# Performance work log

Measured on AMD Instinct MI355X. Metric: run time of the kernel, lower is better.

The kernel has to match this reference:

```python
import jax, jax.numpy as jnp
import numpy as np

N, E, IN, HID, C = 100000, 1600000, 128, 64, 40
LN_EPS = 1e-5


def setup_inputs() -> dict:
    key = jax.random.key(0)
    ks = jax.random.split(key, 20)
    x = jax.random.normal(ks[0], (N, IN), dtype=jnp.float32)
    edge_index = jax.random.randint(ks[1], (2, E), 0, N, dtype=jnp.int64)
    def lin(k, fi, fo):
        s = 1.0 / np.sqrt(fi)
        return jax.random.uniform(k, (fi, fo), jnp.float32, -s, s)
    inp = {"x": x, "edge_index": edge_index}
    dims = [(IN, HID), (HID, HID), (HID, HID)]
    for i, (fi, fo) in enumerate(dims, 1):
        inp[f"W{i}"] = lin(ks[2 * i], fi, fo)
        inp[f"b{i}"] = jnp.zeros((fo,), jnp.float32)
        inp[f"g{i}"] = jnp.ones((fo,), jnp.float32)
        inp[f"t{i}"] = jnp.zeros((fo,), jnp.float32)
    inp["Wf"] = lin(ks[10], HID, C)
    inp["bf"] = jnp.zeros((C,), jnp.float32)
    return inp


def _layer_norm(h, g, t):
    mu = jnp.mean(h, axis=-1, keepdims=True)
    var = jnp.mean((h - mu) ** 2, axis=-1, keepdims=True)
    return g * (h - mu) * jax.lax.rsqrt(var + LN_EPS) + t


def reference(x, edge_index, W1, b1, g1, t1, W2, b2, g2, t2, W3, b3, g3, t3, Wf, bf):
    n = x.shape[0]
    src, dst = edge_index[0], edge_index[1]
    # GCN symmetric normalization (add_self_loops=False): deg = in-degree of dst
    deg = jax.ops.segment_sum(jnp.ones_like(dst, dtype=x.dtype), dst, num_segments=n)
    dinv = jnp.where(deg > 0, jax.lax.rsqrt(deg), 0.0)
    norm = dinv[src] * dinv[dst]  # [E]

    def gcn(h, W, b):
        hw = h @ W                                  # [n, out]
        msg = hw[src] * norm[:, None]               # [E, out] gather + scale
        return jax.ops.segment_sum(msg, dst, num_segments=n) + b

    h = x
    for W, b, g, t in ((W1, b1, g1, t1), (W2, b2, g2, t2), (W3, b3, g3, t3)):
        h = gcn(h, W, b)
        h = _layer_norm(h, g, t)
        h = jax.nn.relu(h)  # dropout is identity in eval mode
    logits = h @ Wf + bf
    return jax.nn.log_softmax(logits, axis=-1)
```

## Files before the change

kernel.cpp:

```cpp
#include <hip/hip_runtime.h>
#include <math.h>
#include <stdint.h>

#define LN_EPS 1e-5f
#define GRP_SHIFT 7
#define MAXBUK 1024
#define PCHUNK 4096

__device__ __forceinline__ unsigned short f2bf(float f) {
  unsigned int u = __float_as_uint(f);
  unsigned int r = u + 0x7fffu + ((u >> 16) & 1u);
  return (unsigned short)(r >> 16);
}
__device__ __forceinline__ float bfLo(unsigned v) { return __uint_as_float(v << 16); }
__device__ __forceinline__ float bfHi(unsigned v) { return __uint_as_float(v & 0xffff0000u); }

__global__ __launch_bounds__(1024) void k_bucket_count(const int* __restrict__ dst,
                                                       int* __restrict__ bcnt, int E, int NB) {
  __shared__ int hist[MAXBUK];
  int t = threadIdx.x;
  for (int i = t; i < NB; i += 1024) hist[i] = 0;
  __syncthreads();
  int e0 = blockIdx.x * PCHUNK;
  int e1 = min(e0 + PCHUNK, E);
#pragma unroll
  for (int j = 0; j < 4; ++j) {
    int i = e0 + t + j * 1024;
    if (i < e1) atomicAdd(&hist[dst[i] >> GRP_SHIFT], 1);
  }
  __syncthreads();
  for (int i = t; i < NB; i += 1024)
    if (hist[i]) atomicAdd(&bcnt[i], hist[i]);
}

__global__ __launch_bounds__(256) void k_bucket_scan(const int* __restrict__ cnt,
                                                     int* __restrict__ base,
                                                     int* __restrict__ cur, int NB) {
  __shared__ int ts[256];
  int t = threadIdx.x;
  int v[4];
  int s = 0;
#pragma unroll
  for (int j = 0; j < 4; ++j) { int i = t * 4 + j; v[j] = (i < NB) ? cnt[i] : 0; s += v[j]; }
  ts[t] = s;
  __syncthreads();
  for (int o = 1; o < 256; o <<= 1) {
    int x = (t >= o) ? ts[t - o] : 0;
    __syncthreads();
    ts[t] += x;
    __syncthreads();
  }
  int run = ts[t] - s;
#pragma unroll
  for (int j = 0; j < 4; ++j) {
    int i = t * 4 + j;
    if (i < NB) { base[i] = run; cur[i] = run; }
    run += v[j];
  }
  if (t == 255) base[NB] = run;
}

__global__ __launch_bounds__(1024) void k_partition(const int* __restrict__ src,
                                                    const int* __restrict__ dst,
                                                    int* __restrict__ bcur,
                                                    unsigned* __restrict__ pairs, int E, int NB) {
  __shared__ int hist[MAXBUK];
  __shared__ int base[MAXBUK];
  int t = threadIdx.x;
  for (int i = t; i < NB; i += 1024) hist[i] = 0;
  __syncthreads();
  int e0 = blockIdx.x * PCHUNK;
  int e1 = min(e0 + PCHUNK, E);
  int sv[4], dv[4], rk[4];
#pragma unroll
  for (int j = 0; j < 4; ++j) {
    int i = e0 + t + j * 1024;
    if (i < e1) {
      sv[j] = src[i];
      dv[j] = dst[i];
      rk[j] = atomicAdd(&hist[dv[j] >> GRP_SHIFT], 1);
    } else {
      dv[j] = -1;
    }
  }
  __syncthreads();
  for (int i = t; i < NB; i += 1024) {
    int c = hist[i];
    base[i] = c ? atomicAdd(&bcur[i], c) : 0;
  }
  __syncthreads();
#pragma unroll
  for (int j = 0; j < 4; ++j) {
    if (dv[j] >= 0) {
      int b = dv[j] >> GRP_SHIFT;
      pairs[base[b] + rk[j]] = ((unsigned)sv[j] << GRP_SHIFT) | (unsigned)(dv[j] & 127);
    }
  }
}

__global__ __launch_bounds__(256) void k_bucket_place(const unsigned* __restrict__ pairs,
                                                      const int* __restrict__ bbase,
                                                      int* __restrict__ offsets,
                                                      float* __restrict__ dinv,
                                                      int* __restrict__ csr, int N, int E) {
  __shared__ int cnt[128];
  __shared__ int sc[128];
  int t = threadIdx.x;
  int b = blockIdx.x;
  int node0 = b << GRP_SHIFT;
  if (t < 128) cnt[t] = 0;
  int beg = bbase[b], end = bbase[b + 1];
  if (b == 0 && t == 0) offsets[N] = E;
  __syncthreads();
  for (int i = beg + t; i < end; i += 256) atomicAdd(&cnt[pairs[i] & 127u], 1);
  __syncthreads();
  if (t < 128) sc[t] = cnt[t];
  __syncthreads();
  for (int o = 1; o < 128; o <<= 1) {
    int x = (t < 128 && t >= o) ? sc[t - o] : 0;
    __syncthreads();
    if (t < 128) sc[t] += x;
    __syncthreads();
  }
  if (t < 128) {
    int excl = sc[t] - cnt[t];
    int node = node0 + t;
    if (node < N) {
      offsets[node] = beg + excl;
      int d = cnt[t];
      dinv[node] = d > 0 ? rsqrtf((float)d) : 0.f;
    }
    sc[t] = beg + excl;
  }
  __syncthreads();
  for (int i = beg + t; i < end; i += 256) {
    unsigned pk = pairs[i];
    int pos = atomicAdd(&sc[pk & 127u], 1);
    csr[pos] = (int)(pk >> GRP_SHIFT);
  }
}

template <int K>
__global__ __launch_bounds__(256) void gemm_scale(const float* __restrict__ A,
                                                  const float* __restrict__ W,
                                                  const float* __restrict__ dinv,
                                                  unsigned short* __restrict__ out, int M) {
  __shared__ float xs[16][64];
  __shared__ float wsh[16][64];
  int t = threadIdx.x;
  int m0 = blockIdx.x * 64;
  int lm = t >> 2;
  int lk = (t & 3) << 2;
  int mr = (t & 15) << 2;
  int cc = (t >> 4) << 2;
  float acc[4][4] = {{0.f}};
  int gm = m0 + lm;
  const bool mok = gm < M;
  for (int kc = 0; kc < K; kc += 16) {
    float4 av = make_float4(0.f, 0.f, 0.f, 0.f);
    if (mok) av = *(const float4*)&A[(size_t)gm * K + kc + lk];
    float wv[4];
#pragma unroll
    for (int r = 0; r < 4; ++r) {
      int k = (t >> 6) + (r << 2);
      wv[r] = W[(size_t)(kc + k) * 64 + (t & 63)];
    }
    __syncthreads();
    xs[lk + 0][lm] = av.x;
    xs[lk + 1][lm] = av.y;
    xs[lk + 2][lm] = av.z;
    xs[lk + 3][lm] = av.w;
#pragma unroll
    for (int r = 0; r < 4; ++r) {
      int k = (t >> 6) + (r << 2);
      wsh[k][t & 63] = wv[r];
    }
    __syncthreads();
#pragma unroll
    for (int k = 0; k < 16; ++k) {
      float4 a4 = *(const float4*)&xs[k][mr];
      float4 b4 = *(const float4*)&wsh[k][cc];
      float a[4] = {a4.x, a4.y, a4.z, a4.w};
      float b[4] = {b4.x, b4.y, b4.z, b4.w};
#pragma unroll
      for (int i = 0; i < 4; ++i)
#pragma unroll
        for (int j = 0; j < 4; ++j) acc[i][j] = fmaf(a[i], b[j], acc[i][j]);
    }
  }
#pragma unroll
  for (int i = 0; i < 4; ++i) {
    int row = m0 + mr + i;
    if (row < M) {
      float sc = dinv[row];
      ushort4 o;
      o.x = f2bf(acc[i][0] * sc);
      o.y = f2bf(acc[i][1] * sc);
      o.z = f2bf(acc[i][2] * sc);
      o.w = f2bf(acc[i][3] * sc);
      *(ushort4*)&out[(size_t)row * 64 + cc] = o;
    }
  }
}

__global__ __launch_bounds__(256) void k_agg(const uint2* __restrict__ hs64,
                                             const int* __restrict__ csr,
                                             const int* __restrict__ offsets,
                                             const float* __restrict__ dinv,
                                             const float* __restrict__ b,
                                             const float* __restrict__ g,
                                             const float* __restrict__ tt,
                                             float* __restrict__ out, int n) {
  int lane = threadIdx.x & 63;
  int q = lane >> 4;
  int fl = lane & 15;
  int node = blockIdx.x * 4 + (threadIdx.x >> 6);
  if (node >= n) return;
  int beg = offsets[node];
  int end = offsets[node + 1];
  float a0 = 0.f, a1 = 0.f, a2 = 0.f, a3 = 0.f;

#define G4U(c)                                                          \
  {                                                                     \
    _Pragma("unroll") for (int j = 0; j < 4; ++j) {                     \
      int sj = __shfl(cs, 16 * (c) + 4 * j + q, 64);                    \
      uint2 v = hs64[(size_t)sj * 16 + fl];                             \
      a0 += bfLo(v.x); a1 += bfHi(v.x);                                 \
      a2 += bfLo(v.y); a3 += bfHi(v.y);                                 \
    }                                                                   \
  }
#define G4M(c)                                                          \
  {                                                                     \
    _Pragma("unroll") for (int j = 0; j < 4; ++j) {                     \
      int sj = __shfl(cs, 16 * (c) + 4 * j + q, 64);                    \
      uint2 v = hs64[(size_t)sj * 16 + fl];                             \
      float m = (e0 + 16 * (c) + 4 * j + q < end) ? 1.f : 0.f;          \
      a0 = fmaf(m, bfLo(v.x), a0);                                      \
      a1 = fmaf(m, bfHi(v.x), a1);                                      \
      a2 = fmaf(m, bfLo(v.y), a2);                                      \
      a3 = fmaf(m, bfHi(v.y), a3);                                      \
    }                                                                   \
  }

  for (int e0 = beg; e0 < end; e0 += 64) {
    int cs = csr[min(e0 + lane, end - 1)];
    int rem = end - e0;
    if (rem >= 64) {
      G4U(0) G4U(1) G4U(2) G4U(3)
    } else {
      int nf = rem >> 4;
      if (nf > 0) G4U(0)
      if (nf > 1) G4U(1)
      if (nf > 2) G4U(2)
      if (rem & 15) {
        switch (nf) {
          case 0: G4M(0) break;
          case 1: G4M(1) break;
          case 2: G4M(2) break;
          default: G4M(3) break;
        }
      }
    }
  }
#undef G4U
#undef G4M

  a0 += __shfl_xor(a0, 16, 64); a0 += __shfl_xor(a0, 32, 64);
  a1 += __shfl_xor(a1, 16, 64); a1 += __shfl_xor(a1, 32, 64);
  a2 += __shfl_xor(a2, 16, 64); a2 += __shfl_xor(a2, 32, 64);
  a3 += __shfl_xor(a3, 16, 64); a3 += __shfl_xor(a3, 32, 64);

  float dv = dinv[node];
  float4 bb = *(const float4*)&b[fl * 4];
  float v0 = fmaf(a0, dv, bb.x);
  float v1 = fmaf(a1, dv, bb.y);
  float v2 = fmaf(a2, dv, bb.z);
  float v3 = fmaf(a3, dv, bb.w);
  float s = v0 + v1 + v2 + v3;
#pragma unroll
  for (int m = 1; m < 16; m <<= 1) s += __shfl_xor(s, m, 64);
  float mu = s * 0.015625f;
  float d0 = v0 - mu, d1 = v1 - mu, d2 = v2 - mu, d3 = v3 - mu;
  float sv = d0 * d0 + d1 * d1 + d2 * d2 + d3 * d3;
#pragma unroll
  for (int m = 1; m < 16; m <<= 1) sv += __shfl_xor(sv, m, 64);
  float rs = rsqrtf(sv * 0.015625f + LN_EPS);
  float4 gg = *(const float4*)&g[fl * 4];
  float4 t4 = *(const float4*)&tt[fl * 4];
  if (q == 0) {
    float4 o;
    o.x = fmaxf(fmaf(gg.x * d0, rs, t4.x), 0.f);
    o.y = fmaxf(fmaf(gg.y * d1, rs, t4.y), 0.f);
    o.z = fmaxf(fmaf(gg.z * d2, rs, t4.z), 0.f);
    o.w = fmaxf(fmaf(gg.w * d3, rs, t4.w), 0.f);
    *(float4*)&out[(size_t)node * 64 + fl * 4] = o;
  }
}

__global__ __launch_bounds__(256) void k_final(const float* __restrict__ h,
                                               const float* __restrict__ Wf,
                                               const float* __restrict__ bf,
                                               float* __restrict__ out, int n) {
  __shared__ float Wl[64 * 40];
  __shared__ float bl[40];
  int t = threadIdx.x;
  for (int i = t; i < 64 * 40; i += 256) Wl[i] = Wf[i];
  if (t < 40) bl[t] = bf[t];
  __syncthreads();
  int n0 = blockIdx.x * 512 + t;
  int n1 = n0 + 256;
  const bool ok0 = n0 < n, ok1 = n1 < n;
  float acc0[40], acc1[40];
#pragma unroll
  for (int c = 0; c < 40; ++c) { acc0[c] = bl[c]; acc1[c] = bl[c]; }
  const float* h0 = &h[(size_t)n0 * 64];
  const float* h1 = &h[(size_t)n1 * 64];
#pragma unroll 2
  for (int k4 = 0; k4 < 16; ++k4) {
    float4 a4 = ok0 ? *(const float4*)&h0[k4 * 4] : make_float4(0.f, 0.f, 0.f, 0.f);
    float4 c4v = ok1 ? *(const float4*)&h1[k4 * 4] : make_float4(0.f, 0.f, 0.f, 0.f);
    float av[4] = {a4.x, a4.y, a4.z, a4.w};
    float bv[4] = {c4v.x, c4v.y, c4v.z, c4v.w};
#pragma unroll
    for (int j = 0; j < 4; ++j) {
      int k = k4 * 4 + j;
#pragma unroll
      for (int c4 = 0; c4 < 10; ++c4) {
        float4 w = *(const float4*)&Wl[k * 40 + c4 * 4];
        acc0[c4 * 4 + 0] = fmaf(av[j], w.x, acc0[c4 * 4 + 0]);
        acc0[c4 * 4 + 1] = fmaf(av[j], w.y, acc0[c4 * 4 + 1]);
        acc0[c4 * 4 + 2] = fmaf(av[j], w.z, acc0[c4 * 4 + 2]);
        acc0[c4 * 4 + 3] = fmaf(av[j], w.w, acc0[c4 * 4 + 3]);
        acc1[c4 * 4 + 0] = fmaf(bv[j], w.x, acc1[c4 * 4 + 0]);
        acc1[c4 * 4 + 1] = fmaf(bv[j], w.y, acc1[c4 * 4 + 1]);
        acc1[c4 * 4 + 2] = fmaf(bv[j], w.z, acc1[c4 * 4 + 2]);
        acc1[c4 * 4 + 3] = fmaf(bv[j], w.w, acc1[c4 * 4 + 3]);
      }
    }
  }
  float m0 = acc0[0], m1 = acc1[0];
#pragma unroll
  for (int c = 1; c < 40; ++c) { m0 = fmaxf(m0, acc0[c]); m1 = fmaxf(m1, acc1[c]); }
  float s0 = 0.f, s1 = 0.f;
#pragma unroll
  for (int c = 0; c < 40; ++c) { s0 += expf(acc0[c] - m0); s1 += expf(acc1[c] - m1); }
  float l0 = m0 + logf(s0);
  float l1 = m1 + logf(s1);
#pragma unroll
  for (int c4 = 0; c4 < 10; ++c4) {
    if (ok0) {
      float4 o = make_float4(acc0[c4 * 4 + 0] - l0, acc0[c4 * 4 + 1] - l0,
                             acc0[c4 * 4 + 2] - l0, acc0[c4 * 4 + 3] - l0);
      *(float4*)&out[(size_t)n0 * 40 + c4 * 4] = o;
    }
    if (ok1) {
      float4 o = make_float4(acc1[c4 * 4 + 0] - l1, acc1[c4 * 4 + 1] - l1,
                             acc1[c4 * 4 + 2] - l1, acc1[c4 * 4 + 3] - l1);
      *(float4*)&out[(size_t)n1 * 40 + c4 * 4] = o;
    }
  }
}

extern "C" void kernel_launch(void* const* d_in, const int* in_sizes, int n_in,
                              void* d_out, int out_size, void* d_ws, size_t ws_size,
                              hipStream_t stream) {
  const float* x  = (const float*)d_in[0];
  const int*   ei = (const int*)d_in[1];
  const float* W1 = (const float*)d_in[2];
  const float* b1 = (const float*)d_in[3];
  const float* g1 = (const float*)d_in[4];
  const float* t1 = (const float*)d_in[5];
  const float* W2 = (const float*)d_in[6];
  const float* b2 = (const float*)d_in[7];
  const float* g2 = (const float*)d_in[8];
  const float* t2 = (const float*)d_in[9];
  const float* W3 = (const float*)d_in[10];
  const float* b3 = (const float*)d_in[11];
  const float* g3 = (const float*)d_in[12];
  const float* t3 = (const float*)d_in[13];
  const float* Wf = (const float*)d_in[14];
  const float* bf = (const float*)d_in[15];
  float* out = (float*)d_out;

  const int N = in_sizes[0] / 128;
  const int E = in_sizes[1] / 2;
  const int* src = ei;
  const int* dst = ei + E;
  const int NBUK = (N + 127) >> GRP_SHIFT;
  const int NEB  = (E + PCHUNK - 1) / PCHUNK;

  char* p = (char*)d_ws;
  auto carve = [&](size_t bytes) -> char* {
    char* r = p;
    p += (bytes + 255) & ~(size_t)255;
    return r;
  };
  int*      bcnt    = (int*)carve((size_t)NBUK * 4);
  int*      bbase   = (int*)carve((size_t)(NBUK + 1) * 4);
  int*      bcur    = (int*)carve((size_t)NBUK * 4);
  unsigned* pairs   = (unsigned*)carve((size_t)E * 4);
  int*      csr     = (int*)carve((size_t)E * 4);
  int*      offsets = (int*)carve((size_t)(N + 1) * 4);
  float*    dinv    = (float*)carve((size_t)N * 4);
  unsigned short* hs = (unsigned short*)carve((size_t)N * 64 * 2);
  float*    hA      = (float*)carve((size_t)N * 64 * 4);
  float*    hB      = (float*)carve((size_t)N * 64 * 4);
  (void)ws_size; (void)n_in; (void)out_size;

  dim3 B(256);
  dim3 B1K(1024);
  hipMemsetAsync(bcnt, 0, (size_t)NBUK * 4, stream);
  k_bucket_count<<<dim3(NEB), B1K, 0, stream>>>(dst, bcnt, E, NBUK);
  k_bucket_scan<<<dim3(1), B, 0, stream>>>(bcnt, bbase, bcur, NBUK);
  k_partition<<<dim3(NEB), B1K, 0, stream>>>(src, dst, bcur, pairs, E, NBUK);
  k_bucket_place<<<dim3(NBUK), B, 0, stream>>>(pairs, bbase, offsets, dinv, csr, N, E);

  const int GB = (N + 63) / 64;
  const int GA = (N + 3) / 4;
  const int GF = (N + 511) / 512;
  gemm_scale<128><<<dim3(GB), B, 0, stream>>>(x, W1, dinv, hs, N);
  k_agg<<<dim3(GA), B, 0, stream>>>((const uint2*)hs, csr, offsets, dinv, b1, g1, t1, hA, N);
  gemm_scale<64><<<dim3(GB), B, 0, stream>>>(hA, W2, dinv, hs, N);
  k_agg<<<dim3(GA), B, 0, stream>>>((const uint2*)hs, csr, offsets, dinv, b2, g2, t2, hB, N);
  gemm_scale<64><<<dim3(GB), B, 0, stream>>>(hB, W3, dinv, hs, N);
  k_agg<<<dim3(GA), B, 0, stream>>>((const uint2*)hs, csr, offsets, dinv, b3, g3, t3, hA, N);
  k_final<<<dim3(GF), B, 0, stream>>>(hA, Wf, bf, out, N);
}
```

Before: 280.3 us.

## Pad CSR rows to 16 with zero-row sentinels and gather via uint4 byte offsets

```diff
diff --git a/kernel.cpp b/kernel.cpp
--- a/kernel.cpp
+++ b/kernel.cpp
@@ -100,21 +100,23 @@
 
 __global__ __launch_bounds__(256) void k_bucket_place(const unsigned* __restrict__ pairs,
                                                       const int* __restrict__ bbase,
-                                                      int* __restrict__ offsets,
+                                                      int* __restrict__ gcur,
+                                                      int2* __restrict__ noff,
                                                       float* __restrict__ dinv,
-                                                      int* __restrict__ csr, int N, int E) {
+                                                      int* __restrict__ csr, int N, int ZOFF) {
   __shared__ int cnt[128];
   __shared__ int sc[128];
+  __shared__ int sbase;
   int t = threadIdx.x;
   int b = blockIdx.x;
   int node0 = b << GRP_SHIFT;
   if (t < 128) cnt[t] = 0;
   int beg = bbase[b], end = bbase[b + 1];
-  if (b == 0 && t == 0) offsets[N] = E;
   __syncthreads();
   for (int i = beg + t; i < end; i += 256) atomicAdd(&cnt[pairs[i] & 127u], 1);
   __syncthreads();
-  if (t < 128) sc[t] = cnt[t];
+  int pcnt = 0;
+  if (t < 128) { pcnt = (cnt[t] + 15) & ~15; sc[t] = pcnt; }
   __syncthreads();
   for (int o = 1; o < 128; o <<= 1) {
     int x = (t < 128 && t >= o) ? sc[t - o] : 0;
@@ -122,21 +124,24 @@
     if (t < 128) sc[t] += x;
     __syncthreads();
   }
+  if (t == 127) sbase = atomicAdd(gcur, sc[127]);
+  __syncthreads();
   if (t < 128) {
-    int excl = sc[t] - cnt[t];
+    int off = sbase + sc[t] - pcnt;
     int node = node0 + t;
     if (node < N) {
-      offsets[node] = beg + excl;
       int d = cnt[t];
+      noff[node] = make_int2(off, off + d);
       dinv[node] = d > 0 ? rsqrtf((float)d) : 0.f;
-    }
-    sc[t] = beg + excl;
+      for (int i = off + d; i < off + pcnt; ++i) csr[i] = ZOFF;
+    }
+    sc[t] = off;
   }
   __syncthreads();
   for (int i = beg + t; i < end; i += 256) {
     unsigned pk = pairs[i];
     int pos = atomicAdd(&sc[pk & 127u], 1);
-    csr[pos] = (int)(pk >> GRP_SHIFT);
+    csr[pos] = (int)(pk & ~127u);
   }
 }
 
@@ -203,9 +208,9 @@
   }
 }
 
-__global__ __launch_bounds__(256) void k_agg(const uint2* __restrict__ hs64,
-                                             const int* __restrict__ csr,
-                                             const int* __restrict__ offsets,
+__global__ __launch_bounds__(256) void k_agg(const char* __restrict__ hsb,
+                                             const uint4* __restrict__ csr4,
+                                             const int2* __restrict__ noff,
                                              const float* __restrict__ dinv,
                                              const float* __restrict__ b,
                                              const float* __restrict__ g,
@@ -216,54 +221,22 @@
   int fl = lane & 15;
   int node = blockIdx.x * 4 + (threadIdx.x >> 6);
   if (node >= n) return;
-  int beg = offsets[node];
-  int end = offsets[node + 1];
+  int2 be = noff[node];
+  int ng = (be.y - be.x + 15) >> 4;
   float a0 = 0.f, a1 = 0.f, a2 = 0.f, a3 = 0.f;
-
-#define G4U(c)                                                          \
-  {                                                                     \
-    _Pragma("unroll") for (int j = 0; j < 4; ++j) {                     \
-      int sj = __shfl(cs, 16 * (c) + 4 * j + q, 64);                    \
-      uint2 v = hs64[(size_t)sj * 16 + fl];                             \
-      a0 += bfLo(v.x); a1 += bfHi(v.x);                                 \
-      a2 += bfLo(v.y); a3 += bfHi(v.y);                                 \
-    }                                                                   \
-  }
-#define G4M(c)                                                          \
-  {                                                                     \
-    _Pragma("unroll") for (int j = 0; j < 4; ++j) {                     \
-      int sj = __shfl(cs, 16 * (c) + 4 * j + q, 64);                    \
-      uint2 v = hs64[(size_t)sj * 16 + fl];                             \
-      float m = (e0 + 16 * (c) + 4 * j + q < end) ? 1.f : 0.f;          \
-      a0 = fmaf(m, bfLo(v.x), a0);                                      \
-      a1 = fmaf(m, bfHi(v.x), a1);                                      \
-      a2 = fmaf(m, bfLo(v.y), a2);                                      \
-      a3 = fmaf(m, bfHi(v.y), a3);                                      \
-    }                                                                   \
-  }
-
-  for (int e0 = beg; e0 < end; e0 += 64) {
-    int cs = csr[min(e0 + lane, end - 1)];
-    int rem = end - e0;
-    if (rem >= 64) {
-      G4U(0) G4U(1) G4U(2) G4U(3)
-    } else {
-      int nf = rem >> 4;
-      if (nf > 0) G4U(0)
-      if (nf > 1) G4U(1)
-      if (nf > 2) G4U(2)
-      if (rem & 15) {
-        switch (nf) {
-          case 0: G4M(0) break;
-          case 1: G4M(1) break;
-          case 2: G4M(2) break;
-          default: G4M(3) break;
-        }
-      }
-    }
-  }
-#undef G4U
-#undef G4M
+  unsigned fo = (unsigned)fl * 8u;
+  int c4 = (be.x >> 2) + q;
+  for (; ng > 0; --ng, c4 += 4) {
+    uint4 iv = csr4[c4];
+    uint2 w0 = *(const uint2*)(hsb + (iv.x + fo));
+    uint2 w1 = *(const uint2*)(hsb + (iv.y + fo));
+    uint2 w2 = *(const uint2*)(hsb + (iv.z + fo));
+    uint2 w3 = *(const uint2*)(hsb + (iv.w + fo));
+    a0 += bfLo(w0.x); a1 += bfHi(w0.x); a2 += bfLo(w0.y); a3 += bfHi(w0.y);
+    a0 += bfLo(w1.x); a1 += bfHi(w1.x); a2 += bfLo(w1.y); a3 += bfHi(w1.y);
+    a0 += bfLo(w2.x); a1 += bfHi(w2.x); a2 += bfLo(w2.y); a3 += bfHi(w2.y);
+    a0 += bfLo(w3.x); a1 += bfHi(w3.x); a2 += bfLo(w3.y); a3 += bfHi(w3.y);
+  }
 
   a0 += __shfl_xor(a0, 16, 64); a0 += __shfl_xor(a0, 32, 64);
   a1 += __shfl_xor(a1, 16, 64); a1 += __shfl_xor(a1, 32, 64);
@@ -276,23 +249,24 @@
   float v1 = fmaf(a1, dv, bb.y);
   float v2 = fmaf(a2, dv, bb.z);
   float v3 = fmaf(a3, dv, bb.w);
-  float s = v0 + v1 + v2 + v3;
-#pragma unroll
-  for (int m = 1; m < 16; m <<= 1) s += __shfl_xor(s, m, 64);
+  float s  = v0 + v1 + v2 + v3;
+  float s2 = fmaf(v0, v0, fmaf(v1, v1, fmaf(v2, v2, v3 * v3)));
+#pragma unroll
+  for (int m = 1; m < 16; m <<= 1) {
+    s  += __shfl_xor(s, m, 64);
+    s2 += __shfl_xor(s2, m, 64);
+  }
   float mu = s * 0.015625f;
-  float d0 = v0 - mu, d1 = v1 - mu, d2 = v2 - mu, d3 = v3 - mu;
-  float sv = d0 * d0 + d1 * d1 + d2 * d2 + d3 * d3;
-#pragma unroll
-  for (int m = 1; m < 16; m <<= 1) sv += __shfl_xor(sv, m, 64);
-  float rs = rsqrtf(sv * 0.015625f + LN_EPS);
+  float var = fmaxf(s2 * 0.015625f - mu * mu, 0.f);
+  float rs = rsqrtf(var + LN_EPS);
   float4 gg = *(const float4*)&g[fl * 4];
   float4 t4 = *(const float4*)&tt[fl * 4];
   if (q == 0) {
     float4 o;
-    o.x = fmaxf(fmaf(gg.x * d0, rs, t4.x), 0.f);
-    o.y = fmaxf(fmaf(gg.y * d1, rs, t4.y), 0.f);
-    o.z = fmaxf(fmaf(gg.z * d2, rs, t4.z), 0.f);
-    o.w = fmaxf(fmaf(gg.w * d3, rs, t4.w), 0.f);
+    o.x = fmaxf(fmaf(gg.x * (v0 - mu), rs, t4.x), 0.f);
+    o.y = fmaxf(fmaf(gg.y * (v1 - mu), rs, t4.y), 0.f);
+    o.z = fmaxf(fmaf(gg.z * (v2 - mu), rs, t4.z), 0.f);
+    o.w = fmaxf(fmaf(gg.w * (v3 - mu), rs, t4.w), 0.f);
     *(float4*)&out[(size_t)node * 64 + fl * 4] = o;
   }
 }
@@ -388,6 +362,7 @@
   const int* dst = ei + E;
   const int NBUK = (N + 127) >> GRP_SHIFT;
   const int NEB  = (E + PCHUNK - 1) / PCHUNK;
+  const int ZOFF = N * 128;
 
   char* p = (char*)d_ws;
   auto carve = [&](size_t bytes) -> char* {
@@ -395,34 +370,36 @@
     p += (bytes + 255) & ~(size_t)255;
     return r;
   };
-  int*      bcnt    = (int*)carve((size_t)NBUK * 4);
+  int*      bcnt    = (int*)carve((size_t)(NBUK + 1) * 4);
+  int*      gcur    = bcnt + NBUK;
   int*      bbase   = (int*)carve((size_t)(NBUK + 1) * 4);
   int*      bcur    = (int*)carve((size_t)NBUK * 4);
   unsigned* pairs   = (unsigned*)carve((size_t)E * 4);
-  int*      csr     = (int*)carve((size_t)E * 4);
-  int*      offsets = (int*)carve((size_t)(N + 1) * 4);
+  int*      csr     = (int*)carve(((size_t)E + 15 * (size_t)N + 256) * 4);
+  int2*     noff    = (int2*)carve((size_t)N * 8);
   float*    dinv    = (float*)carve((size_t)N * 4);
-  unsigned short* hs = (unsigned short*)carve((size_t)N * 64 * 2);
+  unsigned short* hs = (unsigned short*)carve(((size_t)N * 64 + 64) * 2);
   float*    hA      = (float*)carve((size_t)N * 64 * 4);
   float*    hB      = (float*)carve((size_t)N * 64 * 4);
   (void)ws_size; (void)n_in; (void)out_size;
 
   dim3 B(256);
   dim3 B1K(1024);
-  hipMemsetAsync(bcnt, 0, (size_t)NBUK * 4, stream);
+  hipMemsetAsync(bcnt, 0, (size_t)(NBUK + 1) * 4, stream);
+  hipMemsetAsync(hs + (size_t)N * 64, 0, 128, stream);
   k_bucket_count<<<dim3(NEB), B1K, 0, stream>>>(dst, bcnt, E, NBUK);
   k_bucket_scan<<<dim3(1), B, 0, stream>>>(bcnt, bbase, bcur, NBUK);
   k_partition<<<dim3(NEB), B1K, 0, stream>>>(src, dst, bcur, pairs, E, NBUK);
-  k_bucket_place<<<dim3(NBUK), B, 0, stream>>>(pairs, bbase, offsets, dinv, csr, N, E);
+  k_bucket_place<<<dim3(NBUK), B, 0, stream>>>(pairs, bbase, gcur, noff, dinv, csr, N, ZOFF);
 
   const int GB = (N + 63) / 64;
   const int GA = (N + 3) / 4;
   const int GF = (N + 511) / 512;
   gemm_scale<128><<<dim3(GB), B, 0, stream>>>(x, W1, dinv, hs, N);
-  k_agg<<<dim3(GA), B, 0, stream>>>((const uint2*)hs, csr, offsets, dinv, b1, g1, t1, hA, N);
+  k_agg<<<dim3(GA), B, 0, stream>>>((const char*)hs, (const uint4*)csr, noff, dinv, b1, g1, t1, hA, N);
   gemm_scale<64><<<dim3(GB), B, 0, stream>>>(hA, W2, dinv, hs, N);
-  k_agg<<<dim3(GA), B, 0, stream>>>((const uint2*)hs, csr, offsets, dinv, b2, g2, t2, hB, N);
+  k_agg<<<dim3(GA), B, 0, stream>>>((const char*)hs, (const uint4*)csr, noff, dinv, b2, g2, t2, hB, N);
   gemm_scale<64><<<dim3(GB), B, 0, stream>>>(hB, W3, dinv, hs, N);
-  k_agg<<<dim3(GA), B, 0, stream>>>((const uint2*)hs, csr, offsets, dinv, b3, g3, t3, hA, N);
+  k_agg<<<dim3(GA), B, 0, stream>>>((const char*)hs, (const uint4*)csr, noff, dinv, b3, g3, t3, hA, N);
   k_final<<<dim3(GF), B, 0, stream>>>(hA, Wf, bf, out, N);
 }
```

New measurement: 289.9 us. +3.4%, slower.
